# Performance work log

Measured on AMD Instinct MI355X. Metric: run time of the kernel, lower is better.

The kernel has to match this reference:

```python
import jax, jax.numpy as jnp
import numpy as np
import math

# config constants (match init_kwargs)
N_HEAD = 16
KNN_NUM = 4
MEM_FRAC = 4.0
BOOKKEEPING_FRAC = 0.0
RESID_ONLY = False
RESID_FOUND = 0.5   # set_resid_frac(resid_frac): found/current mix
RESID_CURR = 0.5
KNN_INFLUENCE = 1.0
NEG_INF = jnp.finfo(jnp.float32).min


def setup_inputs() -> dict:
    key = jax.random.key(0)
    k1, k2, k3, k4, k5 = jax.random.split(key, 5)
    B, T, C = 1, 2048, 1024
    H, d = N_HEAD, C // N_HEAD
    M = 8192  # per-head memory-store entries
    return {
        "x": jax.random.normal(k1, (B, T, C), jnp.float32),
        "c_attn_w": jax.random.normal(k2, (3 * C, C), jnp.float32) * 0.02,
        "c_proj_w": jax.random.normal(k3, (C, C), jnp.float32) * 0.02,
        "key_store": jax.random.normal(k4, (H, M, d), jnp.float32),
        "value_store": jax.random.normal(k5, (H, M, d), jnp.float32),
    }


def _knn_get(att, k, q, v, key_store, value_store):
    # att: (B,H,T,T), k/q/v: (B,H,T,d), stores: (H,M,d). B must be 1 (original
    # scatter offset i*t is only consistent for b==1).
    B, H, T, d = k.shape
    scale = 1.0 / math.sqrt(d)
    att_last = att[:, :, -1, :]                     # (B,H,T) last-query column
    # bookkeeping_frac == 0.0 -> skipped; mem_frac truthy -> threshold filter
    mask = att_last >= (1.0 / (MEM_FRAC * T))       # nonzero after zeroing

    # per-head flattened token lists, shape (H, N=B*T, d)
    kh = jnp.swapaxes(k, 0, 1).reshape(H, B * T, d)
    qh = jnp.swapaxes(q, 0, 1).reshape(H, B * T, d)
    vh = jnp.swapaxes(v, 0, 1).reshape(H, B * T, d)
    mask_h = jnp.swapaxes(mask, 0, 1).reshape(H, B * T)

    # exact L2 kNN (FAISS IndexFlatL2 equivalent): d2[h,n,m] = ||kh - ks||^2
    d2 = (jnp.sum(kh * kh, -1)[:, :, None]
          - 2.0 * jnp.einsum('hnd,hmd->hnm', kh, key_store)
          + jnp.sum(key_store * key_store, -1)[:, None, :])
    _, idx = jax.lax.top_k(-d2, KNN_NUM)            # (H,N,K) nearest indices

    h_ix = jnp.arange(H)[:, None, None]
    keys_found = key_store[h_ix, idx]               # (H,N,K,d)
    vals_found = value_store[h_ix, idx]
    keys_found = jnp.moveaxis(keys_found, 2, 0)     # (K,H,N,d)
    vals_found = jnp.moveaxis(vals_found, 2, 0)
    if not RESID_ONLY:
        keys_found = jnp.concatenate([kh[None], keys_found], axis=0)  # (K+1,H,N,d)
        vals_found = jnp.concatenate([vh[None], vals_found], axis=0)

    attf = jnp.einsum('khnd,hnd->khn', keys_found, qh) * scale
    attf = jnp.where(jnp.isnan(attf), NEG_INF, attf)
    attf = jax.nn.softmax(attf * KNN_INFLUENCE, axis=0)
    vals_new = jnp.einsum('khn,khnd->hnd', attf, vals_found)
    if RESID_FOUND > 0 or RESID_CURR > 0:
        vals_new = vals_new * RESID_FOUND + vh * RESID_CURR

    v_out = jnp.where(mask_h[..., None], vals_new, vh)   # scatter-equivalent
    return jnp.swapaxes(v_out.reshape(H, B, T, d), 0, 1)  # (B,H,T,d)


def reference(x, c_attn_w, c_proj_w, key_store, value_store):
    B, T, C = x.shape
    H, d = N_HEAD, C // N_HEAD
    qkv = x @ c_attn_w.T                             # (B,T,3C)
    q, k, v = jnp.split(qkv, 3, axis=2)
    q = jnp.swapaxes(q.reshape(B, T, H, d), 1, 2)    # (B,H,T,d)
    k = jnp.swapaxes(k.reshape(B, T, H, d), 1, 2)
    v = jnp.swapaxes(v.reshape(B, T, H, d), 1, 2)

    att = jnp.einsum('bhqd,bhkd->bhqk', q, k) * (1.0 / math.sqrt(d))
    causal = jnp.tril(jnp.ones((T, T), bool))
    att = jnp.where(causal, att, NEG_INF)
    att = jax.nn.softmax(att, axis=-1)

    # knn_get is @torch.no_grad() in the original -> stop_gradient
    v_new = jax.lax.stop_gradient(
        _knn_get(att, k, q, v, key_store, value_store))

    y = jnp.einsum('bhqk,bhkd->bhqd', att, v_new)
    y = jnp.swapaxes(y, 1, 2).reshape(B, T, C)
    return y @ c_proj_w.T
```

## Files before the change

kernel.cpp:

```cpp
#include <hip/hip_runtime.h>
#include <hip/hip_bf16.h>
#include <math.h>

#define TT 2048
#define CC 1024
#define HH 16
#define DDIM 64
#define MM 8192
#define C3 3072
#define SBIAS 256.0f

typedef __bf16 bf16x8 __attribute__((ext_vector_type(8)));
typedef float f32x4 __attribute__((ext_vector_type(4)));

__device__ __forceinline__ float waveReduceSum(float v) {
#pragma unroll
  for (int off = 32; off > 0; off >>= 1) v += __shfl_xor(v, off, 64);
  return v;
}
__device__ __forceinline__ unsigned umn(unsigned a, unsigned b){ return a<b?a:b; }
__device__ __forceinline__ unsigned umed3(unsigned a, unsigned b, unsigned c){
  unsigned d;
  asm("v_med3_u32 %0, %1, %2, %3" : "=v"(d) : "v"(a), "v"(b), "v"(c));
  return d;
}

__device__ __forceinline__ void gload16(const void* g, void* l) {
  __builtin_amdgcn_global_load_lds(
      (const __attribute__((address_space(1))) unsigned int*)g,
      (__attribute__((address_space(3))) unsigned int*)l, 16, 0, 0);
}

__device__ __forceinline__ void conv_split_body(const float* __restrict__ src,
    __hip_bfloat16* __restrict__ hi, __hip_bfloat16* __restrict__ lo, size_t i)
{
  const float4* p = (const float4*)(src + i*8);
  float4 a = p[0], b = p[1];
  float v[8] = {a.x,a.y,a.z,a.w,b.x,b.y,b.z,b.w};
  bf16x8 H, L;
#pragma unroll
  for (int e = 0; e < 8; ++e) {
    __bf16 hb = (__bf16)v[e];
    H[e] = hb;
    L[e] = (__bf16)(v[e] - (float)hb);
  }
  *reinterpret_cast<bf16x8*>(hi + i*8) = H;
  *reinterpret_cast<bf16x8*>(lo + i*8) = L;
}

__device__ __forceinline__ void conv_bf16_body(const float* __restrict__ src,
    __hip_bfloat16* __restrict__ dst, size_t i)
{
  const float4* p = (const float4*)(src + i*8);
  float4 a = p[0], b = p[1];
  float v[8] = {a.x,a.y,a.z,a.w,b.x,b.y,b.z,b.w};
  bf16x8 H;
#pragma unroll
  for (int e = 0; e < 8; ++e) H[e] = (__bf16)v[e];
  *reinterpret_cast<bf16x8*>(dst + i*8) = H;
}

__global__ __launch_bounds__(256) void mega1_k(
    const float* __restrict__ x, __hip_bfloat16* __restrict__ xhi, __hip_bfloat16* __restrict__ xlo,
    const float* __restrict__ wat, __hip_bfloat16* __restrict__ whi, __hip_bfloat16* __restrict__ wlo)
{
  int bid = blockIdx.x;
  if (bid < 1024) conv_split_body(x, xhi, xlo, (size_t)bid*256 + threadIdx.x);
  else            conv_split_body(wat, whi, wlo, (size_t)(bid-1024)*256 + threadIdx.x);
}

__global__ __launch_bounds__(256) void mega2_k(
    const float* __restrict__ qkv, int* __restrict__ mask,
    const float* __restrict__ kst, __hip_bfloat16* __restrict__ ksb,
    float* __restrict__ ksn, float* __restrict__ ksnb,
    __hip_bfloat16* __restrict__ kb,
    const float* __restrict__ wpr, __hip_bfloat16* __restrict__ wprb)
{
  __shared__ float sm[64 + TT + 256];
  const int bid = blockIdx.x;
  const int tid = threadIdx.x;
  if (bid < 16) {
    const int h = bid;
    float* ql = sm;
    float* lg = sm + 64;
    float* red = sm + 64 + TT;
    if (tid < 64) ql[tid] = qkv[(size_t)(TT-1)*C3 + h*DDIM + tid];
    __syncthreads();
    float lmax = -INFINITY;
    for (int t = tid; t < TT; t += 256) {
      const float* kr = qkv + (size_t)t*C3 + CC + h*DDIM;
      float s = 0.f;
#pragma unroll
      for (int d = 0; d < 64; ++d) s += ql[d] * kr[d];
      s *= 0.125f;
      lg[t] = s;
      lmax = fmaxf(lmax, s);
    }
    red[tid] = lmax; __syncthreads();
    for (int off = 128; off > 0; off >>= 1) { if (tid < off) red[tid] = fmaxf(red[tid], red[tid+off]); __syncthreads(); }
    float mx = red[0];
    __syncthreads();
    float ls = 0.f;
    for (int t = tid; t < TT; t += 256) { float e = expf(lg[t]-mx); lg[t] = e; ls += e; }
    red[tid] = ls; __syncthreads();
    for (int off = 128; off > 0; off >>= 1) { if (tid < off) red[tid] += red[tid+off]; __syncthreads(); }
    float Z = red[0];
    for (int t = tid; t < TT; t += 256) mask[h*TT + t] = (lg[t]/Z >= 1.220703125e-4f) ? 1 : 0;
  } else if (bid < 2064) {
    int row = (bid - 16)*64 + (tid >> 2);
    int q = tid & 3;
    const float* src = kst + (size_t)row*64 + q*16;
    float s = 0.f;
    bf16x8 H0, H1;
#pragma unroll
    for (int i = 0; i < 2; ++i) {
      float4 a = ((const float4*)src)[i*2];
      float4 b = ((const float4*)src)[i*2+1];
      s += a.x*a.x + a.y*a.y + a.z*a.z + a.w*a.w
         + b.x*b.x + b.y*b.y + b.z*b.z + b.w*b.w;
      bf16x8 H;
      H[0]=(__bf16)a.x; H[1]=(__bf16)a.y; H[2]=(__bf16)a.z; H[3]=(__bf16)a.w;
      H[4]=(__bf16)b.x; H[5]=(__bf16)b.y; H[6]=(__bf16)b.z; H[7]=(__bf16)b.w;
      if (i == 0) H0 = H; else H1 = H;
    }
    s += __shfl_xor(s, 1, 64);
    s += __shfl_xor(s, 2, 64);
    *reinterpret_cast<bf16x8*>(ksb + (size_t)row*64 + q*16)     = H0;
    *reinterpret_cast<bf16x8*>(ksb + (size_t)row*64 + q*16 + 8) = H1;
    if (q == 0) { ksn[row] = s; ksnb[row] = s + SBIAS; }
  } else if (bid < 3088) {
    int e = (bid - 2064)*256 + tid;
    int dg = e & 7; int t = (e>>3) & (TT-1); int h = e >> 14;
    const float* src = qkv + (size_t)t*C3 + CC + h*64 + dg*8;
    __hip_bfloat16* dst = kb + ((size_t)(h*TT + t)*64 + dg*8);
#pragma unroll
    for (int i = 0; i < 8; ++i) dst[i] = __float2bfloat16(src[i]);
  } else {
    conv_bf16_body(wpr, wprb, (size_t)(bid - 3088)*256 + tid);
  }
}

__global__ __launch_bounds__(256) void vtrans_k(const float* __restrict__ vnew,
    __hip_bfloat16* __restrict__ vbT)
{
  __shared__ float tbuf[64][65];
  const int h = blockIdx.y, t0 = blockIdx.x*64, tid = threadIdx.x;
#pragma unroll
  for (int r = 0; r < 16; ++r) {
    int e = r*256 + tid; int row = e>>6, dv = e&63;
    tbuf[row][dv] = vnew[((size_t)h*TT + t0 + row)*64 + dv];
  }
  __syncthreads();
#pragma unroll
  for (int r = 0; r < 16; ++r) {
    int e = r*256 + tid; int dv = e>>6, tt = e&63;
    vbT[((size_t)h*64 + dv)*TT + t0 + tt] = __float2bfloat16(tbuf[tt][dv]);
  }
}

template<bool SPLIT>
__global__ __launch_bounds__(256) void gemm_mfma_k(
    const __hip_bfloat16* __restrict__ Ah, const __hip_bfloat16* __restrict__ Al,
    const __hip_bfloat16* __restrict__ Bh, const __hip_bfloat16* __restrict__ Bl,
    float* __restrict__ Cc, int M, int N, int K)
{
  __shared__ __align__(16) char lds[2][32768];
  const int tid = threadIdx.x;
  const int nbx = N >> 7;
  const int by = blockIdx.x / nbx, bx = blockIdx.x - by*nbx;
  const int m0 = by << 7, n0 = bx << 7;
  const int w = tid >> 6;
  const int l = tid & 63;
  const int wslot = w << 6;
  const int wi = w >> 1, wj = w & 1;
  const int fr = l & 15, fo = l >> 4;
  const int kw = SPLIT ? 32 : 64;
  const int nsteps = K / kw;

  f32x4 acc[4][4];
#pragma unroll
  for (int i = 0; i < 4; ++i)
#pragma unroll
    for (int j = 0; j < 4; ++j) acc[i][j] = f32x4{0.f,0.f,0.f,0.f};

  int srow[4], schg[4];
#pragma unroll
  for (int r = 0; r < 4; ++r) {
    int s = r*256 + tid;
    srow[r] = s >> 3;
    schg[r] = (s & 7) ^ ((s >> 3) & 7);
  }

  auto stageAB = [&](int buf, int st) {
    const int k0 = st * kw;
#pragma unroll
    for (int r = 0; r < 4; ++r) {
      const __hip_bfloat16 *pa, *pb;
      if (SPLIT) {
        pa = (schg[r] < 4 ? Ah : Al) + (size_t)(m0+srow[r])*K + k0 + (schg[r]&3)*8;
        pb = (schg[r] < 4 ? Bh : Bl) + (size_t)(n0+srow[r])*K + k0 + (schg[r]&3)*8;
      } else {
        pa = Ah + (size_t)(m0+srow[r])*K + k0 + schg[r]*8;
        pb = Bh + (size_t)(n0+srow[r])*K + k0 + schg[r]*8;
      }
      gload16(pa, lds[buf] + (r*256 + wslot)*16);
      gload16(pb, lds[buf] + 16384 + (r*256 + wslot)*16);
    }
  };

  stageAB(0, 0);
  __syncthreads();

  for (int st = 0; st < nsteps; ++st) {
    const int buf = st & 1;
    if (st + 1 < nsteps) stageAB(buf ^ 1, st + 1);
    char* ldsb = lds[buf];

    if (SPLIT) {
      bf16x8 bhf[4], blf[4];
#pragma unroll
      for (int j = 0; j < 4; ++j) {
        int row = wj*64 + j*16 + fr;
        bhf[j] = *(const bf16x8*)(ldsb + 16384 + row*128 + ((fo     ^ (row&7))*16));
        blf[j] = *(const bf16x8*)(ldsb + 16384 + row*128 + (((4+fo) ^ (row&7))*16));
      }
#pragma unroll
      for (int i = 0; i < 4; ++i) {
        int row = wi*64 + i*16 + fr;
        bf16x8 ah = *(const bf16x8*)(ldsb + row*128 + ((fo     ^ (row&7))*16));
        bf16x8 al = *(const bf16x8*)(ldsb + row*128 + (((4+fo) ^ (row&7))*16));
#pragma unroll
        for (int j = 0; j < 4; ++j) {
          acc[i][j] = __builtin_amdgcn_mfma_f32_16x16x32_bf16(al, bhf[j], acc[i][j], 0,0,0);
          acc[i][j] = __builtin_amdgcn_mfma_f32_16x16x32_bf16(ah, blf[j], acc[i][j], 0,0,0);
          acc[i][j] = __builtin_amdgcn_mfma_f32_16x16x32_bf16(ah, bhf[j], acc[i][j], 0,0,0);
        }
      }
    } else {
#pragma unroll
      for (int kk = 0; kk < 2; ++kk) {
        bf16x8 bf[4];
#pragma unroll
        for (int j = 0; j < 4; ++j) {
          int row = wj*64 + j*16 + fr;
          bf[j] = *(const bf16x8*)(ldsb + 16384 + row*128 + (((kk*4+fo) ^ (row&7))*16));
        }
#pragma unroll
        for (int i = 0; i < 4; ++i) {
          int row = wi*64 + i*16 + fr;
          bf16x8 af = *(const bf16x8*)(ldsb + row*128 + (((kk*4+fo) ^ (row&7))*16));
#pragma unroll
          for (int j = 0; j < 4; ++j)
            acc[i][j] = __builtin_amdgcn_mfma_f32_16x16x32_bf16(af, bf[j], acc[i][j], 0,0,0);
        }
      }
    }
    __syncthreads();
  }

  float* ep = (float*)((char*)lds + (size_t)w*8704);
#pragma unroll
  for (int pass = 0; pass < 2; ++pass) {
#pragma unroll
    for (int ii = 0; ii < 2; ++ii) {
      int i = pass*2 + ii;
#pragma unroll
      for (int j = 0; j < 4; ++j)
#pragma unroll
        for (int e = 0; e < 4; ++e)
          ep[(ii*16 + fo*4 + e)*68 + j*16 + fr] = acc[i][j][e];
    }
#pragma unroll
    for (int eidx = 0; eidx < 8; ++eidx) {
      int fi = eidx*64 + l;
      int row = fi >> 4, c4 = fi & 15;
      float4 v4 = *(const float4*)(ep + row*68 + c4*4);
      *(float4*)(Cc + (size_t)(m0 + wi*64 + pass*32 + row)*N + n0 + wj*64 + c4*4) = v4;
    }
  }
}

__global__ __launch_bounds__(256) void knn_chunkmin_k(
    const __hip_bfloat16* __restrict__ kb, const __hip_bfloat16* __restrict__ ksb,
    const float* __restrict__ ksnb, unsigned int* __restrict__ cand)
{
  __shared__ __align__(16) char lds[32768];
  const int tid = threadIdx.x;
  const int bid = blockIdx.x;
  const int orig = (bid & 7)*128 + (bid >> 3);
  const int h  = orig >> 6;
  const int n0 = (orig & 63) * 32;
  const int w  = tid >> 6;
  const int wh = w >> 1;
  const int wr = w & 1;
  const int l  = tid & 63;
  const int cr = l & 15, hi = l >> 4;

  bf16x8 af0, af1;
  {
    const __hip_bfloat16* kbh = kb + (size_t)h*TT*64 + (size_t)(n0 + wr*16 + cr)*64;
    af0 = *reinterpret_cast<const bf16x8*>(kbh + hi*8);
    af1 = *reinterpret_cast<const bf16x8*>(kbh + 32 + hi*8);
  }
  const __hip_bfloat16* ksbh = ksb + (size_t)h*MM*64;
  const float* ksnh = ksnb + (size_t)h*MM;

  char* myhalf = lds + wh*16384;
  int gsrc[4];
#pragma unroll
  for (int r = 0; r < 4; ++r) {
    int s = r*128 + wr*64 + l;
    gsrc[r] = (s & ~7) | ((s & 7) ^ ((s >> 3) & 7));
  }
  const int rb0 = cr*128 + ((hi ^ (l&7))*16);
  const int rb1 = cr*128 + (((4+hi) ^ (l&7))*16);

  unsigned cnd[4][4];
#pragma unroll
  for (int i = 0; i < 4; ++i)
#pragma unroll
    for (int c = 0; c < 4; ++c) cnd[i][c] = 0xFFFFFFFFu;

  auto stage = [&](int buf, int tt) {
    const __hip_bfloat16* src = ksbh + ((size_t)(wh*64 + tt))*4096;
    char* dst = myhalf + buf*8192 + (wr << 10);
#pragma unroll
    for (int r = 0; r < 4; ++r)
      gload16(src + gsrc[r]*8, dst + (r << 11));
  };

  stage(0, 0);
  __syncthreads();

  for (int tt = 0; tt < 64; ++tt) {
    const int buf = tt & 1;
    if (tt + 1 < 64) stage(buf ^ 1, tt + 1);
    char* ldsb = myhalf + buf*8192;
    const int ttg = wh*64 + tt;
    const unsigned crtt = ((unsigned)cr << 7) | (unsigned)ttg;

    float kn0 = ksnh[ttg*64 +  0 + cr];
    float kn1 = ksnh[ttg*64 + 16 + cr];
    float kn2 = ksnh[ttg*64 + 32 + cr];
    float kn3 = ksnh[ttg*64 + 48 + cr];

    f32x4 acc[4];
#pragma unroll
    for (int b = 0; b < 4; ++b) {
      bf16x8 bf0 = *reinterpret_cast<const bf16x8*>(ldsb + b*2048 + rb0);
      bf16x8 bf1 = *reinterpret_cast<const bf16x8*>(ldsb + b*2048 + rb1);
      f32x4 z = {0.f, 0.f, 0.f, 0.f};
      z = __builtin_amdgcn_mfma_f32_16x16x32_bf16(af0, bf0, z, 0, 0, 0);
      z = __builtin_amdgcn_mfma_f32_16x16x32_bf16(af1, bf1, z, 0, 0, 0);
      acc[b] = z;
    }
#pragma unroll
    for (int i = 0; i < 4; ++i) {
      float s0 = fmaf(acc[0][i], -2.f, kn0);
      float s1 = fmaf(acc[1][i], -2.f, kn1);
      float s2 = fmaf(acc[2][i], -2.f, kn2);
      float s3 = fmaf(acc[3][i], -2.f, kn3);
      float m4 = fminf(fminf(s0, s1), fminf(s2, s3));
      unsigned x = (__float_as_uint(m4) & 0xFFFFF800u) | crtt;
      unsigned t0 = umn(cnd[i][0], x);
      unsigned t1 = umed3(x, cnd[i][0], cnd[i][1]);
      unsigned t2 = umed3(x, cnd[i][1], cnd[i][2]);
      unsigned t3 = umed3(x, cnd[i][2], cnd[i][3]);
      cnd[i][0] = t0; cnd[i][1] = t1; cnd[i][2] = t2; cnd[i][3] = t3;
    }
    __syncthreads();
  }

  uint4* sh = (uint4*)lds;
  if (wh == 1) {
#pragma unroll
    for (int i = 0; i < 4; ++i)
      sh[wr*256 + (hi*4+i)*16 + cr] = make_uint4(cnd[i][0], cnd[i][1], cnd[i][2], cnd[i][3]);
  }
  __syncthreads();
  if (wh == 0) {
#pragma unroll
    for (int i = 0; i < 4; ++i) {
      uint4 b = sh[wr*256 + (hi*4+i)*16 + cr];
      int n = n0 + wr*16 + hi*4 + i;
      reinterpret_cast<uint4*>(cand)[(size_t)(h*TT + n)*16 + cr] =
          make_uint4(umn(cnd[i][0], b.w), umn(cnd[i][1], b.z),
                     umn(cnd[i][2], b.y), umn(cnd[i][3], b.x));
    }
  }
}

__global__ __launch_bounds__(256) void knn_fused_k(
    const unsigned int* __restrict__ cand, const float* __restrict__ qkv,
    const float* __restrict__ kstore, const float* __restrict__ vstore,
    const float* __restrict__ ksn, const int* __restrict__ mask,
    float* __restrict__ vnew)
{
  const int row = blockIdx.x*4 + (threadIdx.x>>6);
  const int l = threadIdx.x & 63;
  const int ll = l & 31;
  const int h = row >> 11, t = row & (TT-1);
  const float* base = qkv + (size_t)t*C3 + h*64;
  float vh = base[2*CC + l];
  float* outp = vnew + (size_t)row*64;
  if (!mask[row]) { outp[l] = vh; return; }

  unsigned v = cand[(size_t)row*64 + l];
#pragma unroll
  for (int k = 2; k <= 64; k <<= 1)
#pragma unroll
    for (int j = k>>1; j > 0; j >>= 1) {
      unsigned o = __shfl_xor(v, j, 64);
      bool takeMin = ((l & j) == 0) == ((l & k) == 0);
      v = (takeMin == (o < v)) ? o : v;
    }

  const int c = l >> 1;
  const int b = c & 3;
  unsigned vc = __shfl(v, c >> 2, 64);
  const int m = ((int)(vc & 127u))*64 + b*16 + (int)((vc >> 7) & 15u);
  const int p = l & 1;
  unsigned kh, km;
  {
    const float* kq = base + CC + p*32;
    const float* ksr = kstore + ((size_t)h*MM + m)*64 + p*32;
    float dp = 0.f;
#pragma unroll
    for (int i = 0; i < 8; ++i) {
      float4 a = *(const float4*)(kq + i*4);
      float4 bb = *(const float4*)(ksr + i*4);
      dp = fmaf(a.x,bb.x, fmaf(a.y,bb.y, fmaf(a.z,bb.z, fmaf(a.w,bb.w, dp))));
    }
    dp += __shfl_xor(dp, 1, 64);
    float s = ksn[(size_t)h*MM + m] - 2.f*dp;
    unsigned u = __float_as_uint(s);
    unsigned skey = u ^ (unsigned)(((int)u >> 31) | 0x80000000);
    kh = __shfl(skey, 2*ll, 64);
    km = __shfl((unsigned)m, 2*ll, 64);
#pragma unroll
    for (int k = 2; k <= 32; k <<= 1)
#pragma unroll
      for (int j = k>>1; j > 0; j >>= 1) {
        unsigned oh = __shfl_xor(kh, j, 64);
        unsigned ol = __shfl_xor(km, j, 64);
        bool takeMin = ((ll & j) == 0) == ((ll & k) == 0);
        bool oLess = (oh < kh) || (oh == kh && ol < km);
        if (takeMin == oLess) { kh = oh; km = ol; }
      }
  }

  const int m0 = (int)__shfl(km, 0, 64);
  const int m1 = (int)__shfl(km, 1, 64);
  const int m2 = (int)__shfl(km, 2, 64);
  const int m3 = (int)__shfl(km, 3, 64);
  const int g = l >> 3, gl = l & 7;
  float dq = 0.f;
  if (g < 5) {
    int msel = (g == 0) ? m0 : (g == 1) ? m1 : (g == 2) ? m2 : m3;
    const float* qrow = base + gl*8;
    const float* kr = (g < 4) ? (kstore + ((size_t)h*MM + msel)*64 + gl*8)
                              : (base + CC + gl*8);
    float4 a0 = *(const float4*)(qrow);
    float4 a1 = *(const float4*)(qrow + 4);
    float4 b0 = *(const float4*)(kr);
    float4 b1 = *(const float4*)(kr + 4);
    dq = a0.x*b0.x + a0.y*b0.y + a0.z*b0.z + a0.w*b0.w
       + a1.x*b1.x + a1.y*b1.y + a1.z*b1.z + a1.w*b1.w;
  }
  dq += __shfl_xor(dq, 1, 64);
  dq += __shfl_xor(dq, 2, 64);
  dq += __shfl_xor(dq, 4, 64);
  float d0 = __shfl(dq,  0, 64)*0.125f;
  float d1 = __shfl(dq,  8, 64)*0.125f;
  float d2 = __shfl(dq, 16, 64)*0.125f;
  float d3 = __shfl(dq, 24, 64)*0.125f;
  float d4 = __shfl(dq, 32, 64)*0.125f;
  float mx = fmaxf(fmaxf(fmaxf(d0,d1),fmaxf(d2,d3)),d4);
  float w0 = __expf(d0-mx), w1 = __expf(d1-mx), w2 = __expf(d2-mx),
        w3 = __expf(d3-mx), w4 = __expf(d4-mx);
  float Z = w0+w1+w2+w3+w4;
  float vv = w4*vh
           + w0*vstore[((size_t)h*MM+m0)*64 + l]
           + w1*vstore[((size_t)h*MM+m1)*64 + l]
           + w2*vstore[((size_t)h*MM+m2)*64 + l]
           + w3*vstore[((size_t)h*MM+m3)*64 + l];
  outp[l] = 0.5f*(vv/Z) + 0.5f*vh;
}

__global__ __launch_bounds__(256) void attn_mfma_k(
    const float* __restrict__ qkv, const __hip_bfloat16* __restrict__ kb,
    const __hip_bfloat16* __restrict__ vbT, __hip_bfloat16* __restrict__ yb)
{
  __shared__ __align__(16) char lds[40960];
  const int h = blockIdx.y, bx = blockIdx.x, tid = threadIdx.x;
  const int w = tid>>6, l = tid&63, fr = l&15, fo = l>>4;
  const int wslot = w << 6;
  const __hip_bfloat16* kbh = kb + (size_t)h*TT*64;
  const __hip_bfloat16* vbh = vbT + (size_t)h*64*TT;
  char* Pt = lds + 32768 + w*2048;

  int srow[2], schg[2];
#pragma unroll
  for (int r = 0; r < 2; ++r) {
    int s = r*256 + tid;
    srow[r] = s >> 3;
    schg[r] = (s & 7) ^ ((s >> 3) & 7);
  }

  auto stageKV = [&](int buf, int kt) {
#pragma unroll
    for (int r = 0; r < 2; ++r) {
      gload16(kbh + (size_t)(kt*64 + srow[r])*64 + schg[r]*8,
              lds + buf*16384 + (r*256 + wslot)*16);
      gload16(vbh + (size_t)srow[r]*TT + kt*64 + schg[r]*8,
              lds + buf*16384 + 8192 + (r*256 + wslot)*16);
    }
  };

  for (int half = 0; half < 2; ++half) {
    const int qblk = half ? (31 - bx) : bx;
    const int q0 = qblk * 64;
    bf16x8 qa[2];
    {
      const float* qrow = qkv + (size_t)(q0 + w*16 + fr)*C3 + h*64;
#pragma unroll
      for (int kk = 0; kk < 2; ++kk) {
        float4 u0 = *(const float4*)(qrow + kk*32 + fo*8);
        float4 u1 = *(const float4*)(qrow + kk*32 + fo*8 + 4);
        bf16x8 t;
        t[0]=(__bf16)u0.x; t[1]=(__bf16)u0.y; t[2]=(__bf16)u0.z; t[3]=(__bf16)u0.w;
        t[4]=(__bf16)u1.x; t[5]=(__bf16)u1.y; t[6]=(__bf16)u1.z; t[7]=(__bf16)u1.w;
        qa[kk] = t;
      }
    }
    float mrow[4], lsum[4];
    f32x4 oacc[4];
#pragma unroll
    for (int e = 0; e < 4; ++e) { mrow[e] = -INFINITY; lsum[e] = 0.f; }
#pragma unroll
    for (int jv = 0; jv < 4; ++jv) oacc[jv] = f32x4{0.f,0.f,0.f,0.f};

    const int ntiles = qblk + 1;
    stageKV(0, 0);
    __syncthreads();

    for (int kt = 0; kt < ntiles; ++kt) {
      const int buf = kt & 1;
      if (kt + 1 < ntiles) stageKV(buf ^ 1, kt + 1);
      char* Kt = lds + buf*16384;
      char* Vt = Kt + 8192;

      f32x4 sv[4];
#pragma unroll
      for (int j = 0; j < 4; ++j) {
        int row = j*16 + fr;
        bf16x8 k0f = *(const bf16x8*)(Kt + row*128 + ((fo     ^ (row&7))*16));
        bf16x8 k1f = *(const bf16x8*)(Kt + row*128 + (((4+fo) ^ (row&7))*16));
        f32x4 z = {0.f,0.f,0.f,0.f};
        z = __builtin_amdgcn_mfma_f32_16x16x32_bf16(qa[0], k0f, z, 0,0,0);
        z = __builtin_amdgcn_mfma_f32_16x16x32_bf16(qa[1], k1f, z, 0,0,0);
        sv[j] = z;
      }
      if (kt == qblk) {
#pragma unroll
        for (int j = 0; j < 4; ++j)
#pragma unroll
          for (int e = 0; e < 4; ++e)
            sv[j][e] = (j*16 + fr <= w*16 + fo*4 + e) ? sv[j][e]*0.125f : -INFINITY;
      } else {
#pragma unroll
        for (int j = 0; j < 4; ++j)
#pragma unroll
          for (int e = 0; e < 4; ++e) sv[j][e] *= 0.125f;
      }
      float rmax[4];
#pragma unroll
      for (int e = 0; e < 4; ++e)
        rmax[e] = fmaxf(fmaxf(sv[0][e], sv[1][e]), fmaxf(sv[2][e], sv[3][e]));
#pragma unroll
      for (int off = 1; off < 16; off <<= 1)
#pragma unroll
        for (int e = 0; e < 4; ++e) rmax[e] = fmaxf(rmax[e], __shfl_xor(rmax[e], off, 64));
      float scl[4];
#pragma unroll
      for (int e = 0; e < 4; ++e) {
        float mn = fmaxf(mrow[e], rmax[e]);
        scl[e] = __expf(mrow[e] - mn);
        mrow[e] = mn;
      }
      float rsum[4] = {0.f,0.f,0.f,0.f};
#pragma unroll
      for (int j = 0; j < 4; ++j) {
        int chunkbase = j*2 + (fr>>3);
        int kvoff = (fr&7)*2;
#pragma unroll
        for (int e = 0; e < 4; ++e) {
          float p = __expf(sv[j][e] - mrow[e]);
          rsum[e] += p;
          int qloc = fo*4 + e;
          *(__bf16*)(Pt + qloc*128 + ((chunkbase ^ (qloc&7))*16) + kvoff) = (__bf16)p;
        }
      }
#pragma unroll
      for (int off = 1; off < 16; off <<= 1)
#pragma unroll
        for (int e = 0; e < 4; ++e) rsum[e] += __shfl_xor(rsum[e], off, 64);
#pragma unroll
      for (int e = 0; e < 4; ++e) lsum[e] = lsum[e]*scl[e] + rsum[e];
#pragma unroll
      for (int jv = 0; jv < 4; ++jv)
#pragma unroll
        for (int e = 0; e < 4; ++e) oacc[jv][e] *= scl[e];

      bf16x8 pa0 = *(const bf16x8*)(Pt + fr*128 + ((fo     ^ (fr&7))*16));
      bf16x8 pa1 = *(const bf16x8*)(Pt + fr*128 + (((4+fo) ^ (fr&7))*16));
#pragma unroll
      for (int jv = 0; jv < 4; ++jv) {
        int row = jv*16 + fr;
        bf16x8 v0f = *(const bf16x8*)(Vt + row*128 + ((fo     ^ (row&7))*16));
        bf16x8 v1f = *(const bf16x8*)(Vt + row*128 + (((4+fo) ^ (row&7))*16));
        oacc[jv] = __builtin_amdgcn_mfma_f32_16x16x32_bf16(pa0, v0f, oacc[jv], 0,0,0);
        oacc[jv] = __builtin_amdgcn_mfma_f32_16x16x32_bf16(pa1, v1f, oacc[jv], 0,0,0);
      }
      __syncthreads();
    }
#pragma unroll
    for (int jv = 0; jv < 4; ++jv)
#pragma unroll
      for (int e = 0; e < 4; ++e) {
        int t = q0 + w*16 + fo*4 + e;
        yb[(size_t)t*CC + h*64 + jv*16 + fr] = __float2bfloat16(oacc[jv][e] / lsum[e]);
      }
  }
}

extern "C" void kernel_launch(void* const* d_in, const int* in_sizes, int n_in,
                              void* d_out, int out_size, void* d_ws, size_t ws_size,
                              hipStream_t stream) {
  const float* x   = (const float*)d_in[0];
  const float* wat = (const float*)d_in[1];
  const float* wpr = (const float*)d_in[2];
  const float* kst = (const float*)d_in[3];
  const float* vst = (const float*)d_in[4];
  float* out = (float*)d_out;

  float* ws    = (float*)d_ws;
  float* qkv   = ws;
  float* ksn   = qkv + (size_t)6291456;
  float* ksnb  = ksn + 131072;
  int*   idxb  = (int*)(ksnb + 131072);
  int*   maskb = idxb + 131072;
  __hip_bfloat16* kb = (__hip_bfloat16*)(maskb + 32768);
  float* candRegion = (float*)kb + 1048576;
  unsigned int* candb = (unsigned int*)candRegion;
  float* vnew = candRegion;
  __hip_bfloat16* vbT = (__hip_bfloat16*)(candRegion + 2097152);
  float* split = candRegion + 2097152 + 1048576;
  __hip_bfloat16* xhi = (__hip_bfloat16*)split;
  __hip_bfloat16* xlo = xhi + 2097152;
  __hip_bfloat16* whi = xlo + 2097152;
  __hip_bfloat16* wlo = whi + 3145728;
  __hip_bfloat16* ksb  = (__hip_bfloat16*)split;
  __hip_bfloat16* wprb = ksb + 8388608;
  __hip_bfloat16* yb   = (__hip_bfloat16*)split;

  mega1_k<<<dim3(2560), 256, 0, stream>>>(x, xhi, xlo, wat, whi, wlo);
  gemm_mfma_k<true><<<dim3(16*24), 256, 0, stream>>>(xhi, xlo, whi, wlo, qkv, TT, C3, CC);
  mega2_k<<<dim3(3600), 256, 0, stream>>>(qkv, maskb, kst, ksb, ksn, ksnb, kb, wpr, wprb);
  knn_chunkmin_k<<<dim3(1024), 256, 0, stream>>>(kb, ksb, ksnb, candb);
  knn_fused_k<<<dim3(HH*TT/4), 256, 0, stream>>>(candb, qkv, kst, vst, ksn, maskb, vnew);
  vtrans_k<<<dim3(32, HH), 256, 0, stream>>>(vnew, vbT);
  attn_mfma_k<<<dim3(16, HH), 256, 0, stream>>>(qkv, kb, vbT, yb);
  gemm_mfma_k<false><<<dim3(16*8), 256, 0, stream>>>(yb, nullptr, wprb, nullptr, out, TT, CC, CC);
}
```

Baseline: 290.9 us.

## Split attention KV range across blocks with combine pass; split-K output projection

The attention kernel previously paired two query blocks per workgroup (256 blocks). It now gives each query block two workgroups, each covering half the causal KV range (1024 blocks). Each writes partial outputs plus row max and sum, and a new combine kernel merges them into bf16 y. The output projection GEMM is split along K into two halves and accumulated with atomicAdd into a zeroed output, doubling its grid to 256 blocks. This raises parallelism for both stages. In exchange it adds partial-result traffic, an extra kernel launch, a memset, and float atomics with nondeterministic summation order.

```diff
diff --git a/kernel.cpp b/kernel.cpp
--- a/kernel.cpp
+++ b/kernel.cpp
@@ -158,7 +158,7 @@
   }
 }
 
-template<bool SPLIT>
+template<bool SPLIT, int KSPLIT, bool ATOMIC>
 __global__ __launch_bounds__(256) void gemm_mfma_k(
     const __hip_bfloat16* __restrict__ Ah, const __hip_bfloat16* __restrict__ Al,
     const __hip_bfloat16* __restrict__ Bh, const __hip_bfloat16* __restrict__ Bl,
@@ -167,7 +167,9 @@
   __shared__ __align__(16) char lds[2][32768];
   const int tid = threadIdx.x;
   const int nbx = N >> 7;
-  const int by = blockIdx.x / nbx, bx = blockIdx.x - by*nbx;
+  const int tile = blockIdx.x / KSPLIT;
+  const int ks = blockIdx.x - tile*KSPLIT;
+  const int by = tile / nbx, bx = tile - by*nbx;
   const int m0 = by << 7, n0 = bx << 7;
   const int w = tid >> 6;
   const int l = tid & 63;
@@ -175,7 +177,8 @@
   const int wi = w >> 1, wj = w & 1;
   const int fr = l & 15, fo = l >> 4;
   const int kw = SPLIT ? 32 : 64;
-  const int nsteps = K / kw;
+  const int nsteps = K / kw / KSPLIT;
+  const int k0base = ks * (K / KSPLIT);
 
   f32x4 acc[4][4];
 #pragma unroll
@@ -192,7 +195,7 @@
   }
 
   auto stageAB = [&](int buf, int st) {
-    const int k0 = st * kw;
+    const int k0 = k0base + st * kw;
 #pragma unroll
     for (int r = 0; r < 4; ++r) {
       const __hip_bfloat16 *pa, *pb;
@@ -275,7 +278,13 @@
       int fi = eidx*64 + l;
       int row = fi >> 4, c4 = fi & 15;
       float4 v4 = *(const float4*)(ep + row*68 + c4*4);
-      *(float4*)(Cc + (size_t)(m0 + wi*64 + pass*32 + row)*N + n0 + wj*64 + c4*4) = v4;
+      float* dst = Cc + (size_t)(m0 + wi*64 + pass*32 + row)*N + n0 + wj*64 + c4*4;
+      if (ATOMIC) {
+        atomicAdd(dst+0, v4.x); atomicAdd(dst+1, v4.y);
+        atomicAdd(dst+2, v4.z); atomicAdd(dst+3, v4.w);
+      } else {
+        *(float4*)dst = v4;
+      }
     }
   }
 }
@@ -489,7 +498,8 @@
 
 __global__ __launch_bounds__(256) void attn_mfma_k(
     const float* __restrict__ qkv, const __hip_bfloat16* __restrict__ kb,
-    const __hip_bfloat16* __restrict__ vbT, __hip_bfloat16* __restrict__ yb)
+    const __hip_bfloat16* __restrict__ vbT, float* __restrict__ pso,
+    float2* __restrict__ psml)
 {
   __shared__ __align__(16) char lds[40960];
   const int h = blockIdx.y, bx = blockIdx.x, tid = threadIdx.x;
@@ -517,36 +527,40 @@
     }
   };
 
-  for (int half = 0; half < 2; ++half) {
-    const int qblk = half ? (31 - bx) : bx;
-    const int q0 = qblk * 64;
-    bf16x8 qa[2];
-    {
-      const float* qrow = qkv + (size_t)(q0 + w*16 + fr)*C3 + h*64;
-#pragma unroll
-      for (int kk = 0; kk < 2; ++kk) {
-        float4 u0 = *(const float4*)(qrow + kk*32 + fo*8);
-        float4 u1 = *(const float4*)(qrow + kk*32 + fo*8 + 4);
-        bf16x8 t;
-        t[0]=(__bf16)u0.x; t[1]=(__bf16)u0.y; t[2]=(__bf16)u0.z; t[3]=(__bf16)u0.w;
-        t[4]=(__bf16)u1.x; t[5]=(__bf16)u1.y; t[6]=(__bf16)u1.z; t[7]=(__bf16)u1.w;
-        qa[kk] = t;
-      }
-    }
-    float mrow[4], lsum[4];
-    f32x4 oacc[4];
-#pragma unroll
-    for (int e = 0; e < 4; ++e) { mrow[e] = -INFINITY; lsum[e] = 0.f; }
-#pragma unroll
-    for (int jv = 0; jv < 4; ++jv) oacc[jv] = f32x4{0.f,0.f,0.f,0.f};
-
-    const int ntiles = qblk + 1;
-    stageKV(0, 0);
+  const int n = 31 - (bx >> 1);
+  const int hf = bx & 1;
+  const int c1 = (n + 2) >> 1;
+  const int t0 = hf ? c1 : 0;
+  const int t1 = hf ? (n + 1) : c1;
+  const int q0 = n * 64;
+
+  bf16x8 qa[2];
+  {
+    const float* qrow = qkv + (size_t)(q0 + w*16 + fr)*C3 + h*64;
+#pragma unroll
+    for (int kk = 0; kk < 2; ++kk) {
+      float4 u0 = *(const float4*)(qrow + kk*32 + fo*8);
+      float4 u1 = *(const float4*)(qrow + kk*32 + fo*8 + 4);
+      bf16x8 t;
+      t[0]=(__bf16)u0.x; t[1]=(__bf16)u0.y; t[2]=(__bf16)u0.z; t[3]=(__bf16)u0.w;
+      t[4]=(__bf16)u1.x; t[5]=(__bf16)u1.y; t[6]=(__bf16)u1.z; t[7]=(__bf16)u1.w;
+      qa[kk] = t;
+    }
+  }
+  float mrow[4], lsum[4];
+  f32x4 oacc[4];
+#pragma unroll
+  for (int e = 0; e < 4; ++e) { mrow[e] = -INFINITY; lsum[e] = 0.f; }
+#pragma unroll
+  for (int jv = 0; jv < 4; ++jv) oacc[jv] = f32x4{0.f,0.f,0.f,0.f};
+
+  if (t0 < t1) {
+    stageKV(0, t0);
     __syncthreads();
 
-    for (int kt = 0; kt < ntiles; ++kt) {
-      const int buf = kt & 1;
-      if (kt + 1 < ntiles) stageKV(buf ^ 1, kt + 1);
+    for (int kt = t0; kt < t1; ++kt) {
+      const int buf = (kt - t0) & 1;
+      if (kt + 1 < t1) stageKV(buf ^ 1, kt + 1);
       char* Kt = lds + buf*16384;
       char* Vt = Kt + 8192;
 
@@ -561,7 +575,7 @@
         z = __builtin_amdgcn_mfma_f32_16x16x32_bf16(qa[1], k1f, z, 0,0,0);
         sv[j] = z;
       }
-      if (kt == qblk) {
+      if (kt == n) {
 #pragma unroll
         for (int j = 0; j < 4; ++j)
 #pragma unroll
@@ -624,14 +638,41 @@
       }
       __syncthreads();
     }
-#pragma unroll
-    for (int jv = 0; jv < 4; ++jv)
-#pragma unroll
-      for (int e = 0; e < 4; ++e) {
-        int t = q0 + w*16 + fo*4 + e;
-        yb[(size_t)t*CC + h*64 + jv*16 + fr] = __float2bfloat16(oacc[jv][e] / lsum[e]);
-      }
-  }
+  }
+
+  float* po = pso + ((size_t)hf*HH + h)*32*4096 + (size_t)n*4096;
+  float2* pm = psml + ((size_t)hf*HH + h)*2048 + (size_t)n*64;
+#pragma unroll
+  for (int jv = 0; jv < 4; ++jv)
+#pragma unroll
+    for (int e = 0; e < 4; ++e) {
+      int qloc = w*16 + fo*4 + e;
+      po[qloc*64 + jv*16 + fr] = oacc[jv][e];
+    }
+#pragma unroll
+  for (int e = 0; e < 4; ++e) {
+    if (fr == 0) pm[w*16 + fo*4 + e] = make_float2(mrow[e], lsum[e]);
+  }
+}
+
+__global__ __launch_bounds__(256) void attn_combine_k(
+    const float* __restrict__ pso, const float2* __restrict__ psml,
+    __hip_bfloat16* __restrict__ yb)
+{
+  const int row = blockIdx.x*4 + (threadIdx.x>>6);
+  const int l = threadIdx.x & 63;
+  const int h = row >> 11, t = row & (TT-1);
+  const int n = t >> 6, q = t & 63;
+  size_t ob = ((size_t)h*32 + n)*4096 + (size_t)q*64;
+  size_t mb = ((size_t)h*32 + n)*64 + q;
+  float o1 = pso[ob + l];
+  float o2 = pso[(size_t)HH*32*4096 + ob + l];
+  float2 ml1 = psml[mb];
+  float2 ml2 = psml[(size_t)HH*32*64 + mb];
+  float M = fmaxf(ml1.x, ml2.x);
+  float e1 = __expf(ml1.x - M), e2 = __expf(ml2.x - M);
+  float y = (e1*o1 + e2*o2) / (e1*ml1.y + e2*ml2.y);
+  yb[(size_t)t*CC + h*64 + l] = __float2bfloat16(y);
 }
 
 extern "C" void kernel_launch(void* const* d_in, const int* in_sizes, int n_in,
@@ -654,6 +695,7 @@
   float* candRegion = (float*)kb + 1048576;
   unsigned int* candb = (unsigned int*)candRegion;
   float* vnew = candRegion;
+  __hip_bfloat16* yb = (__hip_bfloat16*)candRegion;
   __hip_bfloat16* vbT = (__hip_bfloat16*)(candRegion + 2097152);
   float* split = candRegion + 2097152 + 1048576;
   __hip_bfloat16* xhi = (__hip_bfloat16*)split;
@@ -662,14 +704,17 @@
   __hip_bfloat16* wlo = whi + 3145728;
   __hip_bfloat16* ksb  = (__hip_bfloat16*)split;
   __hip_bfloat16* wprb = ksb + 8388608;
-  __hip_bfloat16* yb   = (__hip_bfloat16*)split;
+  float* pso  = split;
+  float2* psml = (float2*)(split + 4718592);
 
   mega1_k<<<dim3(2560), 256, 0, stream>>>(x, xhi, xlo, wat, whi, wlo);
-  gemm_mfma_k<true><<<dim3(16*24), 256, 0, stream>>>(xhi, xlo, whi, wlo, qkv, TT, C3, CC);
+  gemm_mfma_k<true,1,false><<<dim3(16*24), 256, 0, stream>>>(xhi, xlo, whi, wlo, qkv, TT, C3, CC);
   mega2_k<<<dim3(3600), 256, 0, stream>>>(qkv, maskb, kst, ksb, ksn, ksnb, kb, wpr, wprb);
   knn_chunkmin_k<<<dim3(1024), 256, 0, stream>>>(kb, ksb, ksnb, candb);
   knn_fused_k<<<dim3(HH*TT/4), 256, 0, stream>>>(candb, qkv, kst, vst, ksn, maskb, vnew);
   vtrans_k<<<dim3(32, HH), 256, 0, stream>>>(vnew, vbT);
-  attn_mfma_k<<<dim3(16, HH), 256, 0, stream>>>(qkv, kb, vbT, yb);
-  gemm_mfma_k<false><<<dim3(16*8), 256, 0, stream>>>(yb, nullptr, wprb, nullptr, out, TT, CC, CC);
-}
+  attn_mfma_k<<<dim3(64, HH), 256, 0, stream>>>(qkv, kb, vbT, pso, psml);
+  attn_combine_k<<<dim3(HH*TT/4), 256, 0, stream>>>(pso, psml, yb);
+  hipMemsetAsync(out, 0, (size_t)out_size*sizeof(float), stream);
+  gemm_mfma_k<false,2,true><<<dim3(256), 256, 0, stream>>>(yb, nullptr, wprb, nullptr, out, TT, CC, CC);
+}
```

Result: slower. 344.3 us (+18.4%).
